# Performance work log

Measured on AMD Instinct MI355X. Metric: run time of the kernel, lower is better.

Reference implementation:

```python
import jax, jax.numpy as jnp
import numpy as np

L = 2          # num_layers
H = 1024       # hidden_size
E = 1024       # embedding_size (== H, required by the feedback matmul)
T = 64         # len(list_desc) decision steps


def setup_inputs() -> dict:
    key = jax.random.key(0)
    ks = jax.random.split(key, 6)
    s = 1.0 / np.sqrt(H)  # keep LSTM gates out of saturation
    return {
        "W_ih": jax.random.normal(ks[0], (L, 4 * H, H), jnp.float32) * s,
        "W_hh": jax.random.normal(ks[1], (L, 4 * H, H), jnp.float32) * s,
        "b_ih": jax.random.normal(ks[2], (L, 4 * H), jnp.float32) * s,
        "b_hh": jax.random.normal(ks[3], (L, 4 * H), jnp.float32) * s,
        "We": jax.random.normal(ks[4], (T, E, H), jnp.float32) * s,
        "be": jax.random.normal(ks[5], (T, E), jnp.float32) * s,
    }


def _lstm_multilayer_step(x, h, c, W_ih, W_hh, b_ih, b_hh):
    # x: [1, E]; h, c: [L, 1, H].  PyTorch gate order: i, f, g, o.
    hs, cs = [], []
    inp = x
    for l in range(L):  # small fixed layer loop
        gates = inp @ W_ih[l].T + b_ih[l] + h[l] @ W_hh[l].T + b_hh[l]  # [1, 4H]
        i, f, g, o = jnp.split(gates, 4, axis=-1)
        c_new = jax.nn.sigmoid(f) * c[l] + jax.nn.sigmoid(i) * jnp.tanh(g)
        h_new = jax.nn.sigmoid(o) * jnp.tanh(c_new)
        hs.append(h_new)
        cs.append(c_new)
        inp = h_new
    return jnp.stack(hs), jnp.stack(cs), inp  # inp = top-layer hidden [1, H]


def reference(W_ih, W_hh, b_ih, b_hh, We, be):
    x0 = jnp.zeros((1, E), jnp.float32)
    h0 = jnp.zeros((L, 1, H), jnp.float32)
    c0 = jnp.zeros((L, 1, H), jnp.float32)

    def step(carry, per_step):
        x, h, c = carry
        We_t, be_t = per_step  # [E, H], [E]
        h, c, top = _lstm_multilayer_step(x, h, c, W_ih, W_hh, b_ih, b_hh)
        logits = top @ We_t.T + be_t            # [1, E]
        decision = jax.nn.softmax(logits, -1)    # [1, E]
        x_next = decision @ We_t                 # [1, H] == [1, E]
        return (x_next, h, c), decision

    _, decisions = jax.lax.scan(step, (x0, h0, c0), (We, be))
    return decisions[:, 0, :]  # [T, E] concatenated decisions
```

## Files before the change

kernel.cpp:

```cpp
#include <hip/hip_runtime.h>

static constexpr int L_ = 2;
static constexpr int H_ = 1024;
static constexpr int E_ = 1024;
static constexpr int T_ = 64;
static constexpr int NB = 256;
static constexpr int BT = 1024;

static constexpr int WS_XV = 0;
static constexpr int WS_H  = WS_XV + (T_ + 1) * H_;
static constexpr int WS_LG = WS_H + T_ * L_ * H_;
static constexpr size_t WS_BYTES = (size_t)(WS_LG + T_ * E_) * 4;

static constexpr unsigned SENT = 0xFFFFFFFFu;

__device__ __forceinline__ float sigm(float v) { return 1.0f / (1.0f + expf(-v)); }

__device__ __forceinline__ unsigned cloadu(const float* p) {
  return __hip_atomic_load((const unsigned*)p, __ATOMIC_RELAXED, __HIP_MEMORY_SCOPE_AGENT);
}
__device__ __forceinline__ void cstore(float* p, float v) {
  __hip_atomic_store(p, v, __ATOMIC_RELAXED, __HIP_MEMORY_SCOPE_AGENT);
}
__device__ __forceinline__ float poll1(const float* p) {
  unsigned v = cloadu(p);
  while (v == SENT) { __builtin_amdgcn_s_sleep(1); v = cloadu(p); }
  return __uint_as_float(v);
}

__global__ __launch_bounds__(BT, 4) void ctrl_kernel(
    const float* __restrict__ W_ih, const float* __restrict__ W_hh,
    const float* __restrict__ b_ih, const float* __restrict__ b_hh,
    const float* __restrict__ We,   const float* __restrict__ be,
    float* __restrict__ out, float* __restrict__ ws)
{
  const int tid  = threadIdx.x;
  const int b    = blockIdx.x;
  const int lane = tid & 63;
  const int w    = tid >> 6;
  const int wl   = w >> 3;
  const int wq   = (w >> 1) & 3;
  const int wh   = w & 1;

  float* xv = ws + WS_XV;
  float* hh = ws + WS_H;
  float* lg = ws + WS_LG;

  const int cswz = ((b & 7) * 32 + (b >> 3)) * 4;

  __shared__ float  s_x[H_];
  __shared__ float  s_gd[2][4][2][4];
  __shared__ float  s_bias[2][4][4];
  __shared__ float  s_be[T_ * 4];
  __shared__ float  s_c[2][4];
  __shared__ float  s_red[16];
  __shared__ float  s_redm[16];
  __shared__ float  s_reds[16];
  __shared__ float4 s_part4[16];

  if (tid < 32) {
    const int l = tid >> 4, q = (tid >> 2) & 3, u = tid & 3;
    const int j = b * 4 + u;
    s_bias[l][q][u] = b_ih[(size_t)l * 4 * H_ + q * H_ + j]
                    + b_hh[(size_t)l * 4 * H_ + q * H_ + j];
  }
  if (tid < 8) s_c[tid >> 2][tid & 3] = 0.0f;
  if (tid < 64) ((float*)s_gd)[tid] = 0.0f;
  if (tid < T_ * 4)
    s_be[tid] = be[(size_t)(tid >> 2) * E_ + b * 4 + (tid & 3)];

  float4 wr[4][4];
  {
    const float* Wbase = (wh == 0) ? W_ih : W_hh;
    #pragma unroll
    for (int u = 0; u < 4; ++u) {
      const size_t row = (size_t)wl * 4 * H_ * H_
                       + ((size_t)wq * H_ + (size_t)(b * 4 + u)) * (size_t)H_;
      #pragma unroll
      for (int m = 0; m < 4; ++m)
        wr[u][m] = *(const float4*)&Wbase[row + (size_t)m * 256 + lane * 4];
    }
  }
  #pragma unroll
  for (int u = 0; u < 4; ++u)
    #pragma unroll
    for (int m = 0; m < 4; ++m)
      asm volatile("" : "+v"(wr[u][m].x), "+v"(wr[u][m].y),
                        "+v"(wr[u][m].z), "+v"(wr[u][m].w));

  auto dot_to = [&](const float4* vin, int dl, int dq, int dh) {
    float a0 = 0.f, a1 = 0.f, a2 = 0.f, a3 = 0.f;
    #pragma unroll
    for (int m = 0; m < 4; ++m) {
      const float4 x4 = vin[m * 64 + lane];
      a0 += wr[0][m].x * x4.x + wr[0][m].y * x4.y + wr[0][m].z * x4.z + wr[0][m].w * x4.w;
      a1 += wr[1][m].x * x4.x + wr[1][m].y * x4.y + wr[1][m].z * x4.z + wr[1][m].w * x4.w;
      a2 += wr[2][m].x * x4.x + wr[2][m].y * x4.y + wr[2][m].z * x4.z + wr[2][m].w * x4.w;
      a3 += wr[3][m].x * x4.x + wr[3][m].y * x4.y + wr[3][m].z * x4.z + wr[3][m].w * x4.w;
    }
    #pragma unroll
    for (int off = 32; off; off >>= 1) {
      a0 += __shfl_down(a0, off, 64);
      a1 += __shfl_down(a1, off, 64);
      a2 += __shfl_down(a2, off, 64);
      a3 += __shfl_down(a3, off, 64);
    }
    if (lane == 0) {
      s_gd[dl][dq][dh][0] = a0; s_gd[dl][dq][dh][1] = a1;
      s_gd[dl][dq][dh][2] = a2; s_gd[dl][dq][dh][3] = a3;
    }
  };

  float4 wlog = *(const float4*)&We[((size_t)(b * 4 + (tid >> 8))) * H_ + (tid & 255) * 4];
  float4 wfb  = *(const float4*)&We[(size_t)tid * H_ + cswz];

  for (int t = 0; t < T_; ++t) {
    if (t == 0) s_x[tid] = 0.0f;
    else        s_x[tid] = poll1(&xv[(size_t)t * H_ + tid]);
    __syncthreads();
    if (wl == 0 && wh == 0) dot_to((const float4*)s_x, 0, wq, 0);
    __syncthreads();
    if (tid < 4) {
      const int u = tid;
      const float g0 = s_gd[0][0][0][u] + s_gd[0][0][1][u] + s_bias[0][0][u];
      const float g1 = s_gd[0][1][0][u] + s_gd[0][1][1][u] + s_bias[0][1][u];
      const float g2 = s_gd[0][2][0][u] + s_gd[0][2][1][u] + s_bias[0][2][u];
      const float g3 = s_gd[0][3][0][u] + s_gd[0][3][1][u] + s_bias[0][3][u];
      const float cn = sigm(g1) * s_c[0][u] + sigm(g0) * tanhf(g2);
      s_c[0][u] = cn;
      cstore(&hh[((size_t)t * L_ + 0) * H_ + b * 4 + u], sigm(g3) * tanhf(cn));
    }

    s_x[tid] = poll1(&hh[((size_t)t * L_ + 0) * H_ + tid]);
    __syncthreads();
    if (wl == 1 && wh == 0) dot_to((const float4*)s_x, 1, wq, 0);
    if (wl == 0 && wh == 1) dot_to((const float4*)s_x, 0, wq, 1);
    __syncthreads();
    if (tid < 4) {
      const int u = tid;
      const float g0 = s_gd[1][0][0][u] + s_gd[1][0][1][u] + s_bias[1][0][u];
      const float g1 = s_gd[1][1][0][u] + s_gd[1][1][1][u] + s_bias[1][1][u];
      const float g2 = s_gd[1][2][0][u] + s_gd[1][2][1][u] + s_bias[1][2][u];
      const float g3 = s_gd[1][3][0][u] + s_gd[1][3][1][u] + s_bias[1][3][u];
      const float cn = sigm(g1) * s_c[1][u] + sigm(g0) * tanhf(g2);
      s_c[1][u] = cn;
      cstore(&hh[((size_t)t * L_ + 1) * H_ + b * 4 + u], sigm(g3) * tanhf(cn));
    }

    s_x[tid] = poll1(&hh[((size_t)t * L_ + 1) * H_ + tid]);
    __syncthreads();
    {
      const float4 h4 = ((const float4*)s_x)[tid & 255];
      float a = wlog.x * h4.x + wlog.y * h4.y + wlog.z * h4.z + wlog.w * h4.w;
      #pragma unroll
      for (int off = 32; off; off >>= 1) a += __shfl_down(a, off, 64);
      if (lane == 0) s_red[w] = a;
    }
    if (wl == 1 && wh == 1) dot_to((const float4*)s_x, 1, wq, 1);
    __syncthreads();
    if (tid < 4) {
      const float v = s_red[tid * 4] + s_red[tid * 4 + 1] + s_red[tid * 4 + 2]
                    + s_red[tid * 4 + 3] + s_be[t * 4 + tid];
      cstore(&lg[(size_t)t * E_ + b * 4 + tid], v);
    }

    s_x[tid] = poll1(&lg[(size_t)t * E_ + tid]);
    __syncthreads();
    {
      const float v = s_x[tid];
      float mm = v;
      #pragma unroll
      for (int off = 32; off; off >>= 1) mm = fmaxf(mm, __shfl_down(mm, off, 64));
      if (lane == 0) s_redm[w] = mm;
      __syncthreads();
      mm = s_redm[0];
      #pragma unroll
      for (int k = 1; k < 16; ++k) mm = fmaxf(mm, s_redm[k]);
      const float ev = expf(v - mm);
      float sv = ev;
      #pragma unroll
      for (int off = 32; off; off >>= 1) sv += __shfl_down(sv, off, 64);
      if (lane == 0) s_reds[w] = sv;
      __syncthreads();
      float ssum = 0.f;
      #pragma unroll
      for (int k = 0; k < 16; ++k) ssum += s_reds[k];
      const float inv = 1.0f / ssum;
      const float d = ev * inv;

      if ((tid >> 2) == b) out[(size_t)t * E_ + tid] = d;

      float4 acc = make_float4(d * wfb.x, d * wfb.y, d * wfb.z, d * wfb.w);
      #pragma unroll
      for (int off = 32; off; off >>= 1) {
        acc.x += __shfl_down(acc.x, off, 64);
        acc.y += __shfl_down(acc.y, off, 64);
        acc.z += __shfl_down(acc.z, off, 64);
        acc.w += __shfl_down(acc.w, off, 64);
      }
      if (lane == 0) s_part4[w] = acc;
      __syncthreads();
      if (tid < 4) {
        float s = 0.f;
        #pragma unroll
        for (int k = 0; k < 16; ++k)
          s += ((const float*)&s_part4[k])[tid];
        cstore(&xv[(size_t)(t + 1) * H_ + cswz + tid], s);
      }
    }

    if (t + 1 < T_) {
      const float* Wn = We + (size_t)(t + 1) * E_ * H_;
      wlog = *(const float4*)&Wn[((size_t)(b * 4 + (tid >> 8))) * H_ + (tid & 255) * 4];
      wfb  = *(const float4*)&Wn[(size_t)tid * H_ + cswz];
    }
  }
}

extern "C" void kernel_launch(void* const* d_in, const int* in_sizes, int n_in,
                              void* d_out, int out_size, void* d_ws, size_t ws_size,
                              hipStream_t stream) {
  const float* W_ih = (const float*)d_in[0];
  const float* W_hh = (const float*)d_in[1];
  const float* b_ih = (const float*)d_in[2];
  const float* b_hh = (const float*)d_in[3];
  const float* We   = (const float*)d_in[4];
  const float* be   = (const float*)d_in[5];
  float* out = (float*)d_out;
  float* ws  = (float*)d_ws;

  (void)hipMemsetAsync(ws, 0xFF, WS_BYTES, stream);

  void* args[] = {(void*)&W_ih, (void*)&W_hh, (void*)&b_ih, (void*)&b_hh,
                  (void*)&We,   (void*)&be,   (void*)&out,  (void*)&ws};
  (void)hipLaunchCooperativeKernel((const void*)ctrl_kernel, dim3(NB), dim3(BT),
                                   args, 0, stream);
}
```

Measured before the change: 992.0 us.

## Pad exchange slots per block and poll them with wide loads

Each block's four published values now sit in their own 64-byte slot in the workspace instead of in a dense array. 256 threads poll one slot each with two 64-bit atomic loads, replacing 1024 threads each polling a scalar. This cuts polling traffic and avoids false sharing between producers. The We prefetch for the next step moves to the upper 512 threads, which stage it in LDS so its load latency overlaps the logits exchange. The cost is more workspace to memset and 32 KB of extra shared memory, which may reduce occupancy.

```diff
diff --git a/kernel.cpp b/kernel.cpp
--- a/kernel.cpp
+++ b/kernel.cpp
@@ -7,25 +7,37 @@
 static constexpr int NB = 256;
 static constexpr int BT = 1024;
 
-static constexpr int WS_XV = 0;
-static constexpr int WS_H  = WS_XV + (T_ + 1) * H_;
-static constexpr int WS_LG = WS_H + T_ * L_ * H_;
-static constexpr size_t WS_BYTES = (size_t)(WS_LG + T_ * E_) * 4;
+static constexpr int SLOT = 16;
+static constexpr int WS_XS = 0;
+static constexpr int WS_HS = WS_XS + (T_ + 1) * NB * SLOT;
+static constexpr int WS_LS = WS_HS + T_ * L_ * NB * SLOT;
+static constexpr size_t WS_BYTES = (size_t)(WS_LS + T_ * NB * SLOT) * 4;
 
 static constexpr unsigned SENT = 0xFFFFFFFFu;
 
 __device__ __forceinline__ float sigm(float v) { return 1.0f / (1.0f + expf(-v)); }
 
-__device__ __forceinline__ unsigned cloadu(const float* p) {
-  return __hip_atomic_load((const unsigned*)p, __ATOMIC_RELAXED, __HIP_MEMORY_SCOPE_AGENT);
-}
 __device__ __forceinline__ void cstore(float* p, float v) {
   __hip_atomic_store(p, v, __ATOMIC_RELAXED, __HIP_MEMORY_SCOPE_AGENT);
 }
-__device__ __forceinline__ float poll1(const float* p) {
-  unsigned v = cloadu(p);
-  while (v == SENT) { __builtin_amdgcn_s_sleep(1); v = cloadu(p); }
-  return __uint_as_float(v);
+__device__ __forceinline__ unsigned long long cload64(const unsigned long long* p) {
+  return __hip_atomic_load(p, __ATOMIC_RELAXED, __HIP_MEMORY_SCOPE_AGENT);
+}
+
+__device__ __forceinline__ float4 poll_slot(const float* slot) {
+  const unsigned long long* p = (const unsigned long long*)slot;
+  unsigned long long a = cload64(p), c = cload64(p + 1);
+  while (((unsigned)a == SENT) | ((unsigned)(a >> 32) == SENT) |
+         ((unsigned)c == SENT) | ((unsigned)(c >> 32) == SENT)) {
+    __builtin_amdgcn_s_sleep(1);
+    a = cload64(p); c = cload64(p + 1);
+  }
+  float4 v;
+  v.x = __uint_as_float((unsigned)a);
+  v.y = __uint_as_float((unsigned)(a >> 32));
+  v.z = __uint_as_float((unsigned)c);
+  v.w = __uint_as_float((unsigned)(c >> 32));
+  return v;
 }
 
 __global__ __launch_bounds__(BT, 4) void ctrl_kernel(
@@ -42,13 +54,15 @@
   const int wq   = (w >> 1) & 3;
   const int wh   = w & 1;
 
-  float* xv = ws + WS_XV;
-  float* hh = ws + WS_H;
-  float* lg = ws + WS_LG;
+  float* XS = ws + WS_XS;
+  float* HS = ws + WS_HS;
+  float* LS = ws + WS_LS;
 
   const int cswz = ((b & 7) * 32 + (b >> 3)) * 4;
 
   __shared__ float  s_x[H_];
+  __shared__ float  s_wlog[4 * H_];
+  __shared__ float  s_wfb[4 * H_];
   __shared__ float  s_gd[2][4][2][4];
   __shared__ float  s_bias[2][4][4];
   __shared__ float  s_be[T_ * 4];
@@ -88,6 +102,16 @@
       asm volatile("" : "+v"(wr[u][m].x), "+v"(wr[u][m].y),
                         "+v"(wr[u][m].z), "+v"(wr[u][m].w));
 
+  const int sidx = tid - 512;
+  float4 r_lg0, r_lg1, r_fb0, r_fb1;
+  if (sidx >= 0) {
+    const int k0 = 2 * sidx, k1 = 2 * sidx + 1;
+    r_lg0 = *(const float4*)&We[((size_t)(b * 4 + (k0 >> 8))) * H_ + (k0 & 255) * 4];
+    r_lg1 = *(const float4*)&We[((size_t)(b * 4 + (k1 >> 8))) * H_ + (k1 & 255) * 4];
+    r_fb0 = *(const float4*)&We[(size_t)k0 * H_ + cswz];
+    r_fb1 = *(const float4*)&We[(size_t)k1 * H_ + cswz];
+  }
+
   auto dot_to = [&](const float4* vin, int dl, int dq, int dh) {
     float a0 = 0.f, a1 = 0.f, a2 = 0.f, a3 = 0.f;
     #pragma unroll
@@ -111,12 +135,20 @@
     }
   };
 
-  float4 wlog = *(const float4*)&We[((size_t)(b * 4 + (tid >> 8))) * H_ + (tid & 255) * 4];
-  float4 wfb  = *(const float4*)&We[(size_t)tid * H_ + cswz];
-
   for (int t = 0; t < T_; ++t) {
-    if (t == 0) s_x[tid] = 0.0f;
-    else        s_x[tid] = poll1(&xv[(size_t)t * H_ + tid]);
+    if (t == 0) {
+      s_x[tid] = 0.0f;
+    } else if (tid < NB) {
+      const float4 v = poll_slot(&XS[((size_t)t * NB + tid) * SLOT]);
+      const int ci = ((tid & 7) * 32 + (tid >> 3)) * 4;
+      *(float4*)&s_x[ci] = v;
+    }
+    if (sidx >= 0) {
+      *(float4*)&s_wlog[(2 * sidx + 0) * 4] = r_lg0;
+      *(float4*)&s_wlog[(2 * sidx + 1) * 4] = r_lg1;
+      *(float4*)&s_wfb[(2 * sidx + 0) * 4]  = r_fb0;
+      *(float4*)&s_wfb[(2 * sidx + 1) * 4]  = r_fb1;
+    }
     __syncthreads();
     if (wl == 0 && wh == 0) dot_to((const float4*)s_x, 0, wq, 0);
     __syncthreads();
@@ -128,10 +160,13 @@
       const float g3 = s_gd[0][3][0][u] + s_gd[0][3][1][u] + s_bias[0][3][u];
       const float cn = sigm(g1) * s_c[0][u] + sigm(g0) * tanhf(g2);
       s_c[0][u] = cn;
-      cstore(&hh[((size_t)t * L_ + 0) * H_ + b * 4 + u], sigm(g3) * tanhf(cn));
-    }
-
-    s_x[tid] = poll1(&hh[((size_t)t * L_ + 0) * H_ + tid]);
+      cstore(&HS[((size_t)(t * L_ + 0) * NB + b) * SLOT + u], sigm(g3) * tanhf(cn));
+    }
+
+    if (tid < NB) {
+      const float4 v = poll_slot(&HS[((size_t)(t * L_ + 0) * NB + tid) * SLOT]);
+      *(float4*)&s_x[tid * 4] = v;
+    }
     __syncthreads();
     if (wl == 1 && wh == 0) dot_to((const float4*)s_x, 1, wq, 0);
     if (wl == 0 && wh == 1) dot_to((const float4*)s_x, 0, wq, 1);
@@ -144,14 +179,18 @@
       const float g3 = s_gd[1][3][0][u] + s_gd[1][3][1][u] + s_bias[1][3][u];
       const float cn = sigm(g1) * s_c[1][u] + sigm(g0) * tanhf(g2);
       s_c[1][u] = cn;
-      cstore(&hh[((size_t)t * L_ + 1) * H_ + b * 4 + u], sigm(g3) * tanhf(cn));
-    }
-
-    s_x[tid] = poll1(&hh[((size_t)t * L_ + 1) * H_ + tid]);
+      cstore(&HS[((size_t)(t * L_ + 1) * NB + b) * SLOT + u], sigm(g3) * tanhf(cn));
+    }
+
+    if (tid < NB) {
+      const float4 v = poll_slot(&HS[((size_t)(t * L_ + 1) * NB + tid) * SLOT]);
+      *(float4*)&s_x[tid * 4] = v;
+    }
     __syncthreads();
     {
-      const float4 h4 = ((const float4*)s_x)[tid & 255];
-      float a = wlog.x * h4.x + wlog.y * h4.y + wlog.z * h4.z + wlog.w * h4.w;
+      const float4 wl4 = *(const float4*)&s_wlog[tid * 4];
+      const float4 h4  = ((const float4*)s_x)[tid & 255];
+      float a = wl4.x * h4.x + wl4.y * h4.y + wl4.z * h4.z + wl4.w * h4.w;
       #pragma unroll
       for (int off = 32; off; off >>= 1) a += __shfl_down(a, off, 64);
       if (lane == 0) s_red[w] = a;
@@ -161,10 +200,21 @@
     if (tid < 4) {
       const float v = s_red[tid * 4] + s_red[tid * 4 + 1] + s_red[tid * 4 + 2]
                     + s_red[tid * 4 + 3] + s_be[t * 4 + tid];
-      cstore(&lg[(size_t)t * E_ + b * 4 + tid], v);
-    }
-
-    s_x[tid] = poll1(&lg[(size_t)t * E_ + tid]);
+      cstore(&LS[((size_t)t * NB + b) * SLOT + tid], v);
+    }
+
+    if (tid < NB) {
+      const float4 v = poll_slot(&LS[((size_t)t * NB + tid) * SLOT]);
+      *(float4*)&s_x[tid * 4] = v;
+    }
+    if (sidx >= 0 && t + 1 < T_) {
+      const float* Wn = We + (size_t)(t + 1) * E_ * H_;
+      const int k0 = 2 * sidx, k1 = 2 * sidx + 1;
+      r_lg0 = *(const float4*)&Wn[((size_t)(b * 4 + (k0 >> 8))) * H_ + (k0 & 255) * 4];
+      r_lg1 = *(const float4*)&Wn[((size_t)(b * 4 + (k1 >> 8))) * H_ + (k1 & 255) * 4];
+      r_fb0 = *(const float4*)&Wn[(size_t)k0 * H_ + cswz];
+      r_fb1 = *(const float4*)&Wn[(size_t)k1 * H_ + cswz];
+    }
     __syncthreads();
     {
       const float v = s_x[tid];
@@ -190,7 +240,8 @@
 
       if ((tid >> 2) == b) out[(size_t)t * E_ + tid] = d;
 
-      float4 acc = make_float4(d * wfb.x, d * wfb.y, d * wfb.z, d * wfb.w);
+      const float4 w4 = *(const float4*)&s_wfb[tid * 4];
+      float4 acc = make_float4(d * w4.x, d * w4.y, d * w4.z, d * w4.w);
       #pragma unroll
       for (int off = 32; off; off >>= 1) {
         acc.x += __shfl_down(acc.x, off, 64);
@@ -205,14 +256,8 @@
         #pragma unroll
         for (int k = 0; k < 16; ++k)
           s += ((const float*)&s_part4[k])[tid];
-        cstore(&xv[(size_t)(t + 1) * H_ + cswz + tid], s);
+        cstore(&XS[((size_t)(t + 1) * NB + b) * SLOT + tid], s);
       }
-    }
-
-    if (t + 1 < T_) {
-      const float* Wn = We + (size_t)(t + 1) * E_ * H_;
-      wlog = *(const float4*)&Wn[((size_t)(b * 4 + (tid >> 8))) * H_ + (tid & 255) * 4];
-      wfb  = *(const float4*)&Wn[(size_t)tid * H_ + cswz];
     }
   }
 }
```

Measured after the change: 1.090 ms. +9.9%, slower.

## Replicate exchange buffers and poll with vectorized 64-bit loads

Applied to the files above, without the earlier changes.

Each producer now writes its values into four replicas of the hidden, logit and feedback exchange buffers, and each block polls the replica chosen by its block index. This spreads contention on the polled cache lines across replicas. Polling also moves from per-thread 32-bit loads to 256 threads each issuing two 64-bit atomic loads for a float4, with a longer sleep between retries. The cost is four times the producer stores and workspace, plus a coarser poll that waits until all four words are ready.

```diff
diff --git a/kernel.cpp b/kernel.cpp
--- a/kernel.cpp
+++ b/kernel.cpp
@@ -6,26 +6,38 @@
 static constexpr int T_ = 64;
 static constexpr int NB = 256;
 static constexpr int BT = 1024;
+static constexpr int R_ = 4;
 
 static constexpr int WS_XV = 0;
-static constexpr int WS_H  = WS_XV + (T_ + 1) * H_;
-static constexpr int WS_LG = WS_H + T_ * L_ * H_;
-static constexpr size_t WS_BYTES = (size_t)(WS_LG + T_ * E_) * 4;
+static constexpr int WS_HH = WS_XV + (T_ + 1) * R_ * H_;
+static constexpr int WS_LG = WS_HH + T_ * L_ * R_ * H_;
+static constexpr size_t WS_BYTES = (size_t)(WS_LG + T_ * R_ * H_) * 4;
 
 static constexpr unsigned SENT = 0xFFFFFFFFu;
 
 __device__ __forceinline__ float sigm(float v) { return 1.0f / (1.0f + expf(-v)); }
 
-__device__ __forceinline__ unsigned cloadu(const float* p) {
-  return __hip_atomic_load((const unsigned*)p, __ATOMIC_RELAXED, __HIP_MEMORY_SCOPE_AGENT);
-}
 __device__ __forceinline__ void cstore(float* p, float v) {
   __hip_atomic_store(p, v, __ATOMIC_RELAXED, __HIP_MEMORY_SCOPE_AGENT);
 }
-__device__ __forceinline__ float poll1(const float* p) {
-  unsigned v = cloadu(p);
-  while (v == SENT) { __builtin_amdgcn_s_sleep(1); v = cloadu(p); }
-  return __uint_as_float(v);
+__device__ __forceinline__ unsigned long long cload64(const unsigned long long* p) {
+  return __hip_atomic_load(p, __ATOMIC_RELAXED, __HIP_MEMORY_SCOPE_AGENT);
+}
+
+__device__ __forceinline__ float4 poll4(const float* p4) {
+  const unsigned long long* p = (const unsigned long long*)p4;
+  unsigned long long a = cload64(p), c = cload64(p + 1);
+  while (((unsigned)a == SENT) | ((unsigned)(a >> 32) == SENT) |
+         ((unsigned)c == SENT) | ((unsigned)(c >> 32) == SENT)) {
+    __builtin_amdgcn_s_sleep(4);
+    a = cload64(p); c = cload64(p + 1);
+  }
+  float4 v;
+  v.x = __uint_as_float((unsigned)a);
+  v.y = __uint_as_float((unsigned)(a >> 32));
+  v.z = __uint_as_float((unsigned)c);
+  v.w = __uint_as_float((unsigned)(c >> 32));
+  return v;
 }
 
 __global__ __launch_bounds__(BT, 4) void ctrl_kernel(
@@ -41,10 +53,11 @@
   const int wl   = w >> 3;
   const int wq   = (w >> 1) & 3;
   const int wh   = w & 1;
-
-  float* xv = ws + WS_XV;
-  float* hh = ws + WS_H;
-  float* lg = ws + WS_LG;
+  const int rg   = b & 3;
+
+  float* XV = ws + WS_XV;
+  float* HH = ws + WS_HH;
+  float* LG = ws + WS_LG;
 
   const int cswz = ((b & 7) * 32 + (b >> 3)) * 4;
 
@@ -115,8 +128,12 @@
   float4 wfb  = *(const float4*)&We[(size_t)tid * H_ + cswz];
 
   for (int t = 0; t < T_; ++t) {
-    if (t == 0) s_x[tid] = 0.0f;
-    else        s_x[tid] = poll1(&xv[(size_t)t * H_ + tid]);
+    if (t == 0) {
+      s_x[tid] = 0.0f;
+    } else if (tid < 256) {
+      const float4 v = poll4(&XV[((size_t)t * R_ + rg) * H_ + 4 * tid]);
+      *(float4*)&s_x[4 * tid] = v;
+    }
     __syncthreads();
     if (wl == 0 && wh == 0) dot_to((const float4*)s_x, 0, wq, 0);
     __syncthreads();
@@ -128,10 +145,16 @@
       const float g3 = s_gd[0][3][0][u] + s_gd[0][3][1][u] + s_bias[0][3][u];
       const float cn = sigm(g1) * s_c[0][u] + sigm(g0) * tanhf(g2);
       s_c[0][u] = cn;
-      cstore(&hh[((size_t)t * L_ + 0) * H_ + b * 4 + u], sigm(g3) * tanhf(cn));
-    }
-
-    s_x[tid] = poll1(&hh[((size_t)t * L_ + 0) * H_ + tid]);
+      const float hv = sigm(g3) * tanhf(cn);
+      #pragma unroll
+      for (int r = 0; r < R_; ++r)
+        cstore(&HH[(((size_t)t * L_ + 0) * R_ + r) * H_ + b * 4 + u], hv);
+    }
+
+    if (tid < 256) {
+      const float4 v = poll4(&HH[(((size_t)t * L_ + 0) * R_ + rg) * H_ + 4 * tid]);
+      *(float4*)&s_x[4 * tid] = v;
+    }
     __syncthreads();
     if (wl == 1 && wh == 0) dot_to((const float4*)s_x, 1, wq, 0);
     if (wl == 0 && wh == 1) dot_to((const float4*)s_x, 0, wq, 1);
@@ -144,10 +167,16 @@
       const float g3 = s_gd[1][3][0][u] + s_gd[1][3][1][u] + s_bias[1][3][u];
       const float cn = sigm(g1) * s_c[1][u] + sigm(g0) * tanhf(g2);
       s_c[1][u] = cn;
-      cstore(&hh[((size_t)t * L_ + 1) * H_ + b * 4 + u], sigm(g3) * tanhf(cn));
-    }
-
-    s_x[tid] = poll1(&hh[((size_t)t * L_ + 1) * H_ + tid]);
+      const float hv = sigm(g3) * tanhf(cn);
+      #pragma unroll
+      for (int r = 0; r < R_; ++r)
+        cstore(&HH[(((size_t)t * L_ + 1) * R_ + r) * H_ + b * 4 + u], hv);
+    }
+
+    if (tid < 256) {
+      const float4 v = poll4(&HH[(((size_t)t * L_ + 1) * R_ + rg) * H_ + 4 * tid]);
+      *(float4*)&s_x[4 * tid] = v;
+    }
     __syncthreads();
     {
       const float4 h4 = ((const float4*)s_x)[tid & 255];
@@ -161,10 +190,15 @@
     if (tid < 4) {
       const float v = s_red[tid * 4] + s_red[tid * 4 + 1] + s_red[tid * 4 + 2]
                     + s_red[tid * 4 + 3] + s_be[t * 4 + tid];
-      cstore(&lg[(size_t)t * E_ + b * 4 + tid], v);
-    }
-
-    s_x[tid] = poll1(&lg[(size_t)t * E_ + tid]);
+      #pragma unroll
+      for (int r = 0; r < R_; ++r)
+        cstore(&LG[((size_t)t * R_ + r) * H_ + b * 4 + tid], v);
+    }
+
+    if (tid < 256) {
+      const float4 v = poll4(&LG[((size_t)t * R_ + rg) * H_ + 4 * tid]);
+      *(float4*)&s_x[4 * tid] = v;
+    }
     __syncthreads();
     {
       const float v = s_x[tid];
@@ -205,7 +239,9 @@
         #pragma unroll
         for (int k = 0; k < 16; ++k)
           s += ((const float*)&s_part4[k])[tid];
-        cstore(&xv[(size_t)(t + 1) * H_ + cswz + tid], s);
+        #pragma unroll
+        for (int r = 0; r < R_; ++r)
+          cstore(&XV[((size_t)(t + 1) * R_ + r) * H_ + cswz + tid], s);
       }
     }
 
```

New measurement: 1.013 ms. 2.1% more time.
